# Kernel tuning notes

Hardware: AMD Instinct MI355X
Metric: run time of the kernel (lower is better)

Reference implementation:

```python
import jax, jax.numpy as jnp
import numpy as np
from jax import lax

B, T, F0 = 16, 1024, 128
L_CNN, L_RNN, D = 3, 3, 512
NF = F0 // 2  # 64, freq dim after stride-2 conv
EPS = 1e-5


def conv2d(x, w, b, stride, pad):
    # x: [B,C,H,W], w: [O,I,kh,kw]
    y = lax.conv_general_dilated(x, w, (stride, stride), [(pad, pad), (pad, pad)],
                                 dimension_numbers=('NCHW', 'OIHW', 'NCHW'))
    return y + b[None, :, None, None]


def ln_last(x, g, b):
    m = x.mean(-1, keepdims=True)
    v = ((x - m) ** 2).mean(-1, keepdims=True)
    return (x - m) * lax.rsqrt(v + EPS) * g + b


def ln_feats(x, g, b):
    # LayerNorm over freq axis (axis 2) of [B,C,F,T] (== transpose(2,3); LN; transpose back)
    m = x.mean(2, keepdims=True)
    v = ((x - m) ** 2).mean(2, keepdims=True)
    return (x - m) * lax.rsqrt(v + EPS) * g[None, None, :, None] + b[None, None, :, None]


def sru_dir(u, x_res, v, b, reverse):
    # u: [T,B,3,D] (candidate, f-pre, r-pre); x_res: [T,B,D] highway input; v,b: [2,D]
    u0 = u[:, :, 0]
    fp = u[:, :, 1] + b[0]
    rp = u[:, :, 2] + b[1]

    def step(c, inp):
        u0t, fpt, rpt, xrt = inp
        f = jax.nn.sigmoid(fpt + v[0] * c)
        r = jax.nn.sigmoid(rpt + v[1] * c)
        c = f * c + (1.0 - f) * u0t
        h = r * jnp.tanh(c) + (1.0 - r) * xrt
        return c, h

    c0 = jnp.zeros(u0.shape[1:], u.dtype)
    _, h = lax.scan(step, c0, (u0, fp, rp, x_res), reverse=reverse)
    return h  # [T,B,D]


def _forward(x, cnn_w, cnn_b, res_w1, res_b1, res_w2, res_b2,
             res_ln1_g, res_ln1_b, res_ln2_g, res_ln2_b,
             proj_w, sru_w, sru_v, sru_b, sru_ln_g, sru_ln_b,
             cls_ln_g, cls_ln_b, cls_w1, cls_b1, cls_w2, cls_b2):
    # stem conv: [B,1,128,1024] -> [B,32,64,512]
    x = conv2d(x, cnn_w, cnn_b, 2, 1)
    # residual CNN blocks (dropout = identity in eval)
    for i in range(L_CNN):
        res = x
        h = jax.nn.relu(ln_feats(x, res_ln1_g[i], res_ln1_b[i]))
        h = conv2d(h, res_w1[i], res_b1[i], 1, 1)
        h = jax.nn.relu(ln_feats(h, res_ln2_g[i], res_ln2_b[i]))
        h = conv2d(h, res_w2[i], res_b2[i], 1, 1)
        x = h + res
    # flatten channels x freq, time-major: [T', B, 32*NF]
    b_, c_, f_, t_ = x.shape
    x = x.reshape(b_, c_ * f_, t_).transpose(2, 0, 1)
    # proj_input_to_hidden_first: 2048 -> 2*D
    x = jnp.einsum('tbi,ih->tbh', x, proj_w)
    # bidirectional SRU layers
    for l in range(L_RNN):
        xl = ln_last(x, sru_ln_g[l], sru_ln_b[l])
        # u: [T,B,dir,gate,D]
        u = jnp.einsum('tbi,idkh->tbdkh', xl, sru_w[l])
        h_f = sru_dir(u[:, :, 0], x[..., :D], sru_v[l, 0], sru_b[l, 0], False)
        h_b = sru_dir(u[:, :, 1], x[..., D:], sru_v[l, 1], sru_b[l, 1], True)
        x = jnp.concatenate([h_f, h_b], axis=-1)
    # classifier: [B, T', 2D] -> [B, T', n_vocab+1]
    x = x.transpose(1, 0, 2)
    x = ln_last(x, cls_ln_g, cls_ln_b)
    x = jax.nn.relu(jnp.einsum('bth,hd->btd', x, cls_w1) + cls_b1)
    x = jnp.einsum('btd,dv->btv', x, cls_w2) + cls_b2
    return x


def setup_inputs() -> dict:
    key = jax.random.key(0)
    ks = iter(jax.random.split(key, 40))

    def rn(shape, s=0.05):
        return jax.random.normal(next(ks), shape, jnp.float32) * s

    return dict(
        x=jax.random.normal(next(ks), (B, 1, F0, T), jnp.float32),
        cnn_w=rn((32, 1, 3, 3)), cnn_b=jnp.zeros(32, jnp.float32),
        res_w1=rn((L_CNN, 32, 32, 3, 3)), res_b1=jnp.zeros((L_CNN, 32), jnp.float32),
        res_w2=rn((L_CNN, 32, 32, 3, 3)), res_b2=jnp.zeros((L_CNN, 32), jnp.float32),
        res_ln1_g=jnp.ones((L_CNN, NF), jnp.float32), res_ln1_b=jnp.zeros((L_CNN, NF), jnp.float32),
        res_ln2_g=jnp.ones((L_CNN, NF), jnp.float32), res_ln2_b=jnp.zeros((L_CNN, NF), jnp.float32),
        proj_w=rn((NF * 32, 2 * D), 0.02),
        sru_w=rn((L_RNN, 2 * D, 2, 3, D), 0.02),
        sru_v=rn((L_RNN, 2, 2, D), 0.1),
        sru_b=jnp.zeros((L_RNN, 2, 2, D), jnp.float32),
        sru_ln_g=jnp.ones((L_RNN, 2 * D), jnp.float32), sru_ln_b=jnp.zeros((L_RNN, 2 * D), jnp.float32),
        cls_ln_g=jnp.ones(2 * D, jnp.float32), cls_ln_b=jnp.zeros(2 * D, jnp.float32),
        cls_w1=rn((2 * D, D), 0.02), cls_b1=jnp.zeros(D, jnp.float32),
        cls_w2=rn((D, 29), 0.02), cls_b2=jnp.zeros(29, jnp.float32),
    )


def reference(x, cnn_w, cnn_b, res_w1, res_b1, res_w2, res_b2,
              res_ln1_g, res_ln1_b, res_ln2_g, res_ln2_b,
              proj_w, sru_w, sru_v, sru_b, sru_ln_g, sru_ln_b,
              cls_ln_g, cls_ln_b, cls_w1, cls_b1, cls_w2, cls_b2):
    return _forward(x, cnn_w, cnn_b, res_w1, res_b1, res_w2, res_b2,
                    res_ln1_g, res_ln1_b, res_ln2_g, res_ln2_b,
                    proj_w, sru_w, sru_v, sru_b, sru_ln_g, sru_ln_b,
                    cls_ln_g, cls_ln_b, cls_w1, cls_b1, cls_w2, cls_b2)
```

## Files before the change

kernel.cpp:

```cpp
#include <hip/hip_runtime.h>

typedef unsigned short u16;
typedef unsigned int u32;
typedef __attribute__((ext_vector_type(8))) short short8;
typedef __attribute__((ext_vector_type(4))) float floatx4;

__device__ __forceinline__ float bf2f(u16 u) {
    union { unsigned int i; float f; } v; v.i = ((unsigned int)u) << 16; return v.f;
}
__device__ __forceinline__ u16 f2bf(float f) {
    union { float f; unsigned int i; } v; v.f = f;
    unsigned int i = v.i + 0x7fffu + ((v.i >> 16) & 1u);
    return (u16)(i >> 16);
}

#define GLL(g, l) __builtin_amdgcn_global_load_lds( \
    (const __attribute__((address_space(1))) void*)(g), \
    (__attribute__((address_space(3))) void*)(l), 16, 0, 0)

#define WAITVM(n) asm volatile("s_waitcnt vmcnt(" #n ")" ::: "memory")
#define SBAR() __builtin_amdgcn_sched_barrier(0)

#define HA_BSTRIDE 1085568

__global__ __launch_bounds__(256) void sniff_k(const u16* __restrict__ x, int* __restrict__ flag) {
    __shared__ int red[4];
    int cnt = 0;
    for (int i = 0; i < 16; ++i) {
        u16 v = x[(threadIdx.x * 16 + i) * 2];
        int e = (v >> 7) & 0xFF;
        if (e >= 110 && e <= 135) cnt++;
    }
    #pragma unroll
    for (int off = 32; off; off >>= 1) cnt += __shfl_down(cnt, off);
    if ((threadIdx.x & 63) == 0) red[threadIdx.x >> 6] = cnt;
    __syncthreads();
    if (threadIdx.x == 0) {
        int tot = red[0] + red[1] + red[2] + red[3];
        *flag = (tot < 2048) ? 1 : 0;
    }
}

__device__ __forceinline__ float ldin(const void* p, size_t i, int isf32) {
    return isf32 ? ((const float*)p)[i] : bf2f(((const u16*)p)[i]);
}

struct CvtArgs {
    const void* src[19];
    int len[19];
    int off[19];
};
__global__ __launch_bounds__(256) void cvtall_k(CvtArgs a, float* __restrict__ dst,
                                                const int* __restrict__ flag) {
    int isf32 = *flag;
    int seg = blockIdx.y;
    int n = a.len[seg];
    const void* s = a.src[seg];
    float* d = dst + a.off[seg];
    for (int i = blockIdx.x * 256 + threadIdx.x; i < n; i += gridDim.x * 256)
        d[i] = ldin(s, i, isf32);
}

__global__ __launch_bounds__(256) void wtr_k(const void* __restrict__ W, int ldw, size_t wofs,
                                             u16* __restrict__ Wt, int ldt,
                                             const int* __restrict__ flag) {
    int isf32 = *flag;
    __shared__ u16 t[64][65];
    int k0 = blockIdx.x * 64, n0 = blockIdx.y * 64;
    int tid = threadIdx.x;
    #pragma unroll
    for (int i = 0; i < 16; ++i) {
        int kk = i * 4 + (tid >> 6), nn = tid & 63;
        t[kk][nn] = f2bf(ldin(W, wofs + (size_t)(k0 + kk) * ldw + n0 + nn, isf32));
    }
    __syncthreads();
    #pragma unroll
    for (int i = 0; i < 16; ++i) {
        int nn = i * 4 + (tid >> 6), kk = tid & 63;
        Wt[(size_t)(n0 + nn) * ldt + k0 + kk] = t[kk][nn];
    }
}

__global__ __launch_bounds__(256) void zero_k(float4* __restrict__ p, int n4) {
    float4 z = {0.f, 0.f, 0.f, 0.f};
    for (int i = blockIdx.x * 256 + threadIdx.x; i < n4; i += gridDim.x * 256) p[i] = z;
}
__global__ __launch_bounds__(256) void fill_k(float* __restrict__ p, int n) {
    int i = blockIdx.x * 256 + threadIdx.x;
    if (i < n) p[i] = 1.0e6f;
}

__global__ __launch_bounds__(256) void conv1_k(const void* __restrict__ x, const float* __restrict__ w,
                                               const float* __restrict__ bias, float* __restrict__ out,
                                               const int* __restrict__ flag) {
    int isf32 = *flag;
    int idx = blockIdx.x * 256 + threadIdx.x;
    int t  = idx & 511;
    int f  = (idx >> 9) & 63;
    int cg = (idx >> 15) & 7;
    int b  = idx >> 18;
    size_t xb = (size_t)b * 128 * 1024;

    float wr[4][9];
    #pragma unroll
    for (int i = 0; i < 4; ++i)
        #pragma unroll
        for (int k = 0; k < 9; ++k) wr[i][k] = w[(cg * 4 + i) * 9 + k];

    float acc[4];
    #pragma unroll
    for (int i = 0; i < 4; ++i) acc[i] = bias[cg * 4 + i];

    #pragma unroll
    for (int df = 0; df < 3; ++df) {
        int fi = 2 * f + df - 1;
        if (fi < 0 || fi >= 128) continue;
        size_t rowb = xb + (size_t)fi * 1024;
        float xv[3];
        #pragma unroll
        for (int dt = 0; dt < 3; ++dt) {
            int ti = 2 * t + dt - 1;
            float v = 0.f;
            if (ti >= 0 && ti < 1024) v = ldin(x, rowb + ti, isf32);
            xv[dt] = v;
        }
        #pragma unroll
        for (int i = 0; i < 4; ++i)
            #pragma unroll
            for (int dt = 0; dt < 3; ++dt)
                acc[i] = fmaf(wr[i][df * 3 + dt], xv[dt], acc[i]);
    }
    size_t obase = (((size_t)b * 32 + cg * 4) * 64 + f) * 512 + t;
    #pragma unroll
    for (int i = 0; i < 4; ++i) out[obase + (size_t)i * 64 * 512] = acc[i];
}

__global__ __launch_bounds__(256) void stats_k(const void* __restrict__ X, int isbf,
                                               float* __restrict__ sm, float* __restrict__ sr) {
    int idx = blockIdx.x * 256 + threadIdx.x;
    int t  = idx & 511;
    int bc = idx >> 9;
    size_t base = (size_t)bc * 64 * 512 + t;
    float s = 0.f, s2 = 0.f;
    #pragma unroll 8
    for (int f = 0; f < 64; ++f) {
        float v = isbf ? bf2f(((const u16*)X)[base + f * 512]) : ((const float*)X)[base + f * 512];
        s += v; s2 += v * v;
    }
    float m  = s * (1.f / 64.f);
    float var = fmaxf(s2 * (1.f / 64.f) - m * m, 0.f);
    sm[idx] = m;
    sr[idx] = rsqrtf(var + 1e-5f);
}

__global__ __launch_bounds__(256) void apply_k(const void* __restrict__ in, int isbf,
                                               const float* __restrict__ sm, const float* __restrict__ sr,
                                               const float* __restrict__ g, const float* __restrict__ be,
                                               u16* __restrict__ Ha) {
    int f = blockIdx.x;
    int b = blockIdx.y;
    float gg = g[f], bb_ = be[f];
    for (int it = 0; it < 2; ++it) {
        int t = it * 256 + threadIdx.x;
        u32 pk[16];
        #pragma unroll
        for (int cp = 0; cp < 16; ++cp) {
            u32 w = 0;
            #pragma unroll
            for (int half = 0; half < 2; ++half) {
                int ci = cp * 2 + half;
                size_t xi = (((size_t)b * 32 + ci) * 64 + f) * 512 + t;
                float xv = isbf ? bf2f(((const u16*)in)[xi]) : ((const float*)in)[xi];
                int si = (b * 32 + ci) * 512 + t;
                float hv = fmaxf((xv - sm[si]) * sr[si] * gg + bb_, 0.f);
                w |= ((u32)f2bf(hv)) << (half * 16);
            }
            pk[cp] = w;
        }
        u32* orow = (u32*)(Ha + (size_t)b * HA_BSTRIDE + ((size_t)(f + 1) * 514 + (t + 1)) * 32);
        #pragma unroll
        for (int q = 0; q < 16; ++q) orow[q] = pk[q];
    }
}

#define CVL 4
__global__ __launch_bounds__(256) void convm_k(const u16* __restrict__ Ha, void* __restrict__ out,
                                               const float* __restrict__ w, const float* __restrict__ bias,
                                               const float* __restrict__ res) {
    __shared__ __align__(16) u16 act[2][1536 * 8];
    int F0    = blockIdx.x * 16;
    int tbase = blockIdx.y * 64;
    int b     = blockIdx.z;
    const u16* Hb = Ha + (size_t)b * HA_BSTRIDE;
    int tid  = threadIdx.x;
    int lane = tid & 63;
    int wv   = tid >> 6;
    int quad = lane >> 4;
    int r    = lane & 15;
    int hasres = (res != nullptr);

    int ufp[6], utp[6], uq[6];
    #pragma unroll
    for (int it = 0; it < 6; ++it) {
        int u = it * 256 + tid;
        int u2 = (u < 1296) ? u : (u - 1296);
        int fp = u2 / 72;
        int rem = u2 - fp * 72;
        ufp[it] = fp; utp[it] = rem >> 2; uq[it] = rem & 3;
    }

    auto stage = [&](int tile, int bw) {
        int t00 = tbase + tile * 16;
        #pragma unroll
        for (int it = 0; it < 6; ++it) {
            int u = it * 256 + tid;
            GLL(Hb + ((size_t)(F0 + ufp[it]) * 514 + (t00 + utp[it])) * 32 + uq[it] * 8,
                &act[bw][u * 8]);
        }
    };

    short8 bfrag[3][3][2];
    #pragma unroll
    for (int df = 0; df < 3; ++df)
        #pragma unroll
        for (int dt = 0; dt < 3; ++dt)
            #pragma unroll
            for (int ct = 0; ct < 2; ++ct) {
                short8 v;
                #pragma unroll
                for (int j = 0; j < 8; ++j) {
                    int co = ct * 16 + r, ci = quad * 8 + j;
                    v[j] = (short)f2bf(w[(co * 32 + ci) * 9 + df * 3 + dt]);
                }
                bfrag[df][dt][ct] = v;
            }

    WAITVM(0);
    SBAR();
    stage(0, 0);
    SBAR();

    int fb = wv * 4;
    #pragma unroll 1
    for (int i = 0; i < CVL; ++i) {
        if (i < CVL - 1) stage(i + 1, (i + 1) & 1);
        SBAR();
        if (i == 0)            { WAITVM(6); }
        else if (i < CVL - 1)  { if (hasres) WAITVM(22); else WAITVM(14); }
        else                   { if (hasres) WAITVM(16); else WAITVM(8); }
        SBAR();
        __builtin_amdgcn_s_barrier();
        SBAR();

        const u16* ab = act[i & 1];
        floatx4 acc[4][2];
        #pragma unroll
        for (int ii = 0; ii < 4; ++ii)
            #pragma unroll
            for (int j = 0; j < 2; ++j)
                #pragma unroll
                for (int k = 0; k < 4; ++k) acc[ii][j][k] = 0.f;

        #pragma unroll
        for (int fh = 0; fh < 6; ++fh) {
            short8 af[3];
            #pragma unroll
            for (int dt = 0; dt < 3; ++dt)
                af[dt] = *(const short8*)&ab[((fb + fh) * 18 + (r + dt)) * 32 + quad * 8];
            #pragma unroll
            for (int df = 0; df < 3; ++df) {
                int rel = fh - df;
                if (rel < 0 || rel >= 4) continue;
                #pragma unroll
                for (int dt = 0; dt < 3; ++dt)
                    #pragma unroll
                    for (int ct = 0; ct < 2; ++ct)
                        acc[rel][ct] = __builtin_amdgcn_mfma_f32_16x16x32_bf16(
                            af[dt], bfrag[df][dt][ct], acc[rel][ct], 0, 0, 0);
            }
        }

        int t0 = tbase + i * 16;
        int tt = t0 + quad * 4;
        #pragma unroll
        for (int rel = 0; rel < 4; ++rel)
            #pragma unroll
            for (int ct = 0; ct < 2; ++ct) {
                int f  = F0 + fb + rel;
                int co = ct * 16 + r;
                size_t base = (((size_t)b * 32 + co) * 64 + f) * 512 + tt;
                float bs = bias[co];
                if (hasres) {
                    float4 rv = *(const float4*)(res + base);
                    float4 o;
                    o.x = acc[rel][ct][0] + bs + rv.x;
                    o.y = acc[rel][ct][1] + bs + rv.y;
                    o.z = acc[rel][ct][2] + bs + rv.z;
                    o.w = acc[rel][ct][3] + bs + rv.w;
                    *(float4*)((float*)out + base) = o;
                } else {
                    ushort4 o;
                    o.x = f2bf(acc[rel][ct][0] + bs);
                    o.y = f2bf(acc[rel][ct][1] + bs);
                    o.z = f2bf(acc[rel][ct][2] + bs);
                    o.w = f2bf(acc[rel][ct][3] + bs);
                    *(ushort4*)((u16*)out + base) = o;
                }
            }
        SBAR();
        __builtin_amdgcn_s_barrier();
        SBAR();
    }
}

__global__ __launch_bounds__(256) void transpose_k(const float* __restrict__ X, u16* __restrict__ A) {
    __shared__ float tile[64][65];
    int t0 = blockIdx.x * 64;
    int c  = blockIdx.y;
    int b  = blockIdx.z;
    const float* p = X + (((size_t)b * 32 + c) * 64) * 512 + t0;
    #pragma unroll
    for (int i = 0; i < 16; ++i) {
        int f = i * 4 + (threadIdx.x >> 6);
        int t = threadIdx.x & 63;
        tile[f][t] = p[(size_t)f * 512 + t];
    }
    __syncthreads();
    #pragma unroll
    for (int i = 0; i < 16; ++i) {
        int t = i * 4 + (threadIdx.x >> 6);
        int f = threadIdx.x & 63;
        A[((size_t)(t0 + t) * 16 + b) * 2048 + c * 64 + f] = f2bf(tile[f][t]);
    }
}

__global__ __launch_bounds__(256) void lnlast_k(const float* __restrict__ X, u16* __restrict__ Y,
                                                const float* __restrict__ g, const float* __restrict__ bt,
                                                int width) {
    int row = blockIdx.x;
    const float* p = X + (size_t)row * width;
    float s = 0.f, s2 = 0.f;
    for (int i = threadIdx.x; i < width; i += 256) { float v = p[i]; s += v; s2 += v * v; }
    #pragma unroll
    for (int off = 32; off; off >>= 1) { s += __shfl_down(s, off); s2 += __shfl_down(s2, off); }
    __shared__ float red[4][2];
    int wv = threadIdx.x >> 6;
    if ((threadIdx.x & 63) == 0) { red[wv][0] = s; red[wv][1] = s2; }
    __syncthreads();
    if (threadIdx.x == 0) {
        float a = 0.f, b2 = 0.f;
        for (int i = 0; i < 4; ++i) { a += red[i][0]; b2 += red[i][1]; }
        float m = a / width;
        float var = fmaxf(b2 / width - m * m, 0.f);
        red[0][0] = m; red[0][1] = rsqrtf(var + 1e-5f);
    }
    __syncthreads();
    float m = red[0][0], rs = red[0][1];
    u16* q = Y + (size_t)row * width;
    for (int i = threadIdx.x; i < width; i += 256)
        q[i] = f2bf((p[i] - m) * rs * g[i] + bt[i]);
}

__global__ __launch_bounds__(256) void gemm_bt(const u16* __restrict__ A, const u16* __restrict__ A2,
                                               int lda, const u16* __restrict__ Bt, int ldb,
                                               void* __restrict__ C, void* __restrict__ C2,
                                               int ldc, int nsplit,
                                               const float* __restrict__ bias, int relu, int K,
                                               int obf) {
    __shared__ u16 As[128 * 32];
    __shared__ u16 Bs[128 * 32];
    int tid  = threadIdx.x;
    int bm   = blockIdx.x * 128;
    int bn   = blockIdx.y * 128;
    const u16* Ab = A;
    void* Cb = C;
    int cn = bn;
    if (bn >= nsplit) { Ab = A2; Cb = C2; cn = bn - nsplit; }

    int lane = tid & 63;
    int wv   = tid >> 6;
    int quad = lane >> 4;
    int r    = lane & 15;
    int wm   = (wv >> 1) * 64;
    int wn   = (wv & 1) * 64;

    floatx4 acc[4][4];
    #pragma unroll
    for (int i = 0; i < 4; ++i)
        #pragma unroll
        for (int j = 0; j < 4; ++j)
            #pragma unroll
            for (int k = 0; k < 4; ++k) acc[i][j][k] = 0.f;

    int row0 = tid >> 2;
    int ks0  = ((tid & 3) ^ ((tid >> 3) & 3)) * 8;
    const u16* Abase  = Ab + (size_t)(bm + row0) * lda + ks0;
    const u16* Abase2 = Ab + (size_t)(bm + 64 + row0) * lda + ks0;
    const u16* Bbase  = Bt + (size_t)(bn + row0) * ldb + ks0;
    const u16* Bbase2 = Bt + (size_t)(bn + 64 + row0) * ldb + ks0;
    u16* AsD  = As + tid * 8;
    u16* AsD2 = As + 2048 + tid * 8;
    u16* BsD  = Bs + tid * 8;
    u16* BsD2 = Bs + 2048 + tid * 8;

    for (int k0 = 0; k0 < K; k0 += 32) {
        GLL(Abase + k0, AsD);
        GLL(Abase2 + k0, AsD2);
        GLL(Bbase + k0, BsD);
        GLL(Bbase2 + k0, BsD2);
        __syncthreads();
        int col = (quad ^ ((r >> 1) & 3)) * 8;
        short8 af[4], bf[4];
        #pragma unroll
        for (int mi = 0; mi < 4; ++mi) af[mi] = *(const short8*)&As[(wm + mi * 16 + r) * 32 + col];
        #pragma unroll
        for (int ni = 0; ni < 4; ++ni) bf[ni] = *(const short8*)&Bs[(wn + ni * 16 + r) * 32 + col];
        #pragma unroll
        for (int mi = 0; mi < 4; ++mi)
            #pragma unroll
            for (int ni = 0; ni < 4; ++ni)
                acc[mi][ni] = __builtin_amdgcn_mfma_f32_16x16x32_bf16(af[mi], bf[ni], acc[mi][ni], 0, 0, 0);
        __syncthreads();
    }

    #pragma unroll
    for (int mi = 0; mi < 4; ++mi)
        #pragma unroll
        for (int ni = 0; ni < 4; ++ni) {
            int col = cn + wn + ni * 16 + r;
            float bs = bias ? bias[col] : 0.f;
            #pragma unroll
            for (int reg = 0; reg < 4; ++reg) {
                int row = bm + wm + mi * 16 + quad * 4 + reg;
                float v = acc[mi][ni][reg] + bs;
                if (relu) v = fmaxf(v, 0.f);
                if (obf) ((u16*)Cb)[(size_t)row * ldc + col] = f2bf(v);
                else     ((float*)Cb)[(size_t)row * ldc + col] = v;
            }
        }
}

#define TC 256
__global__ __launch_bounds__(64) void scan_k(const u16* __restrict__ Uf, const u16* __restrict__ Ub,
                                             const float* __restrict__ Xp, float* __restrict__ Xn,
                                             float* __restrict__ cstate, const float* __restrict__ vv,
                                             const float* __restrict__ bb, int t0f, int t0b, int init) {
    __shared__ __align__(16) char lds[4][10240];
    int tid = threadIdx.x;
    int d   = blockIdx.x >> 7;
    int idx = blockIdx.x & 127;
    int b   = idx >> 3;
    int h0  = (idx & 7) * 64;
    int h   = h0 + tid;
    int gid = d * 8192 + idx * 64 + tid;

    float v0 = vv[(d * 2 + 0) * 512 + h];
    float v1 = vv[(d * 2 + 1) * 512 + h];
    float b0 = bb[(d * 2 + 0) * 512 + h];
    float b1 = bb[(d * 2 + 1) * 512 + h];
    const u16* U = d ? Ub : Uf;
    int t0 = d ? t0b : t0f;
    float* ob = Xn + (size_t)b * 1024 + d * 512 + h;
    float cc = init ? 0.f : cstate[gid];
    int tstp = d ? -16384 : 16384;

    const char* gp[10];
    int dlt[10];
    #pragma unroll
    for (int it = 0; it < 10; ++it) {
        int u = it * 64 + tid;
        int s = u / 40;
        int j = u - s * 40;
        int sl0 = d ? (TC - 1 - s) : s;
        if (j < 24) {
            int k = j >> 3, jj = j & 7;
            gp[it] = (const char*)(U + ((size_t)(sl0 * 16 + b) * 1536 + k * 512 + h0 + jj * 8));
            dlt[it] = d ? -786432 : 786432;
        } else {
            gp[it] = (const char*)(Xp + ((size_t)(t0 + sl0) * 16384 + (size_t)b * 1024 + d * 512 + h0 + (j - 24) * 4));
            dlt[it] = d ? -1048576 : 1048576;
        }
    }
    char* lbase = (char*)&lds[0][0] + tid * 16;
    auto stage = [&](int bw) {
        char* lb = lbase + bw * 10240;
        #pragma unroll
        for (int it = 0; it < 10; ++it) {
            GLL(gp[it], lb + it * 1024);
            gp[it] += dlt[it];
        }
    };

    asm volatile("s_waitcnt vmcnt(0)" ::: "memory");
    SBAR();
    stage(0);
    stage(1);
    stage(2);
    SBAR();

    #pragma unroll 1
    for (int tk = 0; tk < 16; ++tk) {
        switch (tk) {
            case 0:  WAITVM(20); break;
            case 1:  WAITVM(36); break;
            case 14: WAITVM(42); break;
            case 15: WAITVM(32); break;
            default: WAITVM(52); break;
        }
        SBAR();
        const char* Bb = (const char*)&lds[0][0] + (size_t)(tk & 3) * 10240;
        float* op = ob + (size_t)(t0 + (d ? (TC - 1 - tk * 16) : tk * 16)) * 16384;
        #pragma unroll
        for (int s = 0; s < 16; ++s) {
            const char* sb = Bb + s * 640;
            float u0 = bf2f(*(const u16*)(sb + tid * 2));
            float fp = bf2f(*(const u16*)(sb + 128 + tid * 2)) + b0;
            float rp = bf2f(*(const u16*)(sb + 256 + tid * 2)) + b1;
            float xr = *(const float*)(sb + 384 + tid * 4);
            float f = 1.f / (1.f + __expf(-(fp + v0 * cc)));
            float r = 1.f / (1.f + __expf(-(rp + v1 * cc)));
            cc = f * cc + (1.f - f) * u0;
            float th = 1.f - 2.f / (__expf(2.f * cc) + 1.f);
            *op = r * th + (1.f - r) * xr;
            op += tstp;
        }
        SBAR();
        if (tk < 13) stage((tk + 3) & 3);
        SBAR();
    }
    cstate[gid] = cc;
}

__global__ __launch_bounds__(256) void cls2_k(const float* __restrict__ FC1, const float* __restrict__ W2,
                                              const float* __restrict__ b2, void* __restrict__ out,
                                              const int* __restrict__ flag) {
    int isf32 = *flag;
    int tid = threadIdx.x;
    int rh = tid >> 7;
    int ks = (tid >> 5) & 3;
    int v  = tid & 31;
    int row = blockIdx.x * 2 + rh;
    const float* p = FC1 + (size_t)row * 512 + ks * 128;
    const float* wp = W2 + (size_t)ks * 128 * 29;
    float acc = 0.f;
    #pragma unroll 4
    for (int k = 0; k < 128; ++k) {
        float wv = (v < 29) ? wp[k * 29 + v] : 0.f;
        acc = fmaf(p[k], wv, acc);
    }
    acc += __shfl_xor(acc, 32);
    __shared__ float red[2][2][32];
    if ((tid & 63) < 32) red[rh][(tid >> 6) & 1][v] = acc;
    __syncthreads();
    if ((tid & 127) < 32 && v < 29) {
        float s = red[rh][0][v] + red[rh][1][v] + b2[v];
        int t = row >> 4, b = row & 15;
        size_t oi = ((size_t)b * 512 + t) * 29 + v;
        if (isf32) ((float*)out)[oi] = s;
        else       ((u16*)out)[oi]   = f2bf(s);
    }
}

extern "C" void kernel_launch(void* const* d_in, const int* in_sizes, int n_in,
                              void* d_out, int out_size, void* d_ws, size_t ws_size,
                              hipStream_t stream) {
    const void* x      = d_in[0];
    const void* proj_w = d_in[11];
    const void* sru_w  = d_in[12];
    const void* cls_w1 = d_in[19];

    float* ws = (float*)d_ws;
    const size_t O_X    = 0;
    const size_t O_C    = 16777216;
    const size_t O_HA   = 25165824;
    const size_t O_SM   = 33850368;
    const size_t O_SR   = 34112512;
    const size_t O_CST  = 34374656;
    const size_t O_PARK = 34391040;
    const size_t O_FLAG = 34483488;
    const size_t TOTAL  = 34483504;
    if (ws_size < TOTAL * sizeof(float)) {
        fill_k<<<(out_size + 255) / 256, 256, 0, stream>>>((float*)d_out, out_size);
        return;
    }

    float* X   = ws + O_X;
    u16*   C   = (u16*)(ws + O_C);
    u16*   HA  = (u16*)(ws + O_HA);
    float* SM  = ws + O_SM;
    float* SR  = ws + O_SR;
    float* CST = ws + O_CST;
    float* PK  = ws + O_PARK;
    int*   FLG = (int*)(ws + O_FLAG);

    u16*   Abf = (u16*)(ws + O_C);
    u16*   BtP = (u16*)(ws + 0);
    float* XP0 = ws + 25165824;
    u16*   XL  = (u16*)(ws + 0);
    float* XP1 = ws + 4194304;
    u16*   Uf  = (u16*)(ws + 12582912);
    u16*   Ub  = (u16*)(ws + 15728640);
    u16*   BtS = (u16*)(ws + 18874368);
    u16*   BtC = (u16*)(ws + O_SM);
    float* FC1 = ws + 12582912;

    float* p_cnn_w = PK + 0;      float* p_cnn_b = PK + 288;
    float* p_rw1   = PK + 320;    float* p_rb1   = PK + 27968;
    float* p_rw2   = PK + 28064;  float* p_rb2   = PK + 55712;
    float* p_l1g   = PK + 55808;  float* p_l1b   = PK + 56000;
    float* p_l2g   = PK + 56192;  float* p_l2b   = PK + 56384;
    float* p_sv    = PK + 56576;  float* p_sb    = PK + 62720;
    float* p_slng  = PK + 68864;  float* p_slnb  = PK + 71936;
    float* p_clng  = PK + 75008;  float* p_clnb  = PK + 76032;
    float* p_cb1   = PK + 77056;  float* p_cw2   = PK + 77568;
    float* p_cb2   = PK + 92416;

    sniff_k<<<1, 256, 0, stream>>>((const u16*)x, FLG);

    CvtArgs ca;
    const int srcidx[19] = {1,2,3,4,5,6,7,8,9,10,13,14,15,16,17,18,20,21,22};
    const int lens[19]   = {288,32,27648,96,27648,96,192,192,192,192,6144,6144,3072,3072,1024,1024,512,14848,29};
    const int offs[19]   = {0,288,320,27968,28064,55712,55808,56000,56192,56384,56576,62720,68864,71936,75008,76032,77056,77568,92416};
    for (int i = 0; i < 19; ++i) { ca.src[i] = d_in[srcidx[i]]; ca.len[i] = lens[i]; ca.off[i] = offs[i]; }
    cvtall_k<<<dim3(108, 19), 256, 0, stream>>>(ca, PK, FLG);

    zero_k<<<2048, 256, 0, stream>>>((float4*)HA, 2171136);
    conv1_k<<<16384, 256, 0, stream>>>(x, p_cnn_w, p_cnn_b, X, FLG);

    for (int i = 0; i < 3; ++i) {
        stats_k<<<1024, 256, 0, stream>>>(X, 0, SM, SR);
        apply_k<<<dim3(64, 16), 256, 0, stream>>>(X, 0, SM, SR, p_l1g + i * 64, p_l1b + i * 64, HA);
        convm_k<<<dim3(4, 8, 16), 256, 0, stream>>>(HA, C, p_rw1 + i * 9216, p_rb1 + i * 32, nullptr);
        stats_k<<<1024, 256, 0, stream>>>(C, 1, SM, SR);
        apply_k<<<dim3(64, 16), 256, 0, stream>>>(C, 1, SM, SR, p_l2g + i * 64, p_l2b + i * 64, HA);
        convm_k<<<dim3(4, 8, 16), 256, 0, stream>>>(HA, X, p_rw2 + i * 9216, p_rb2 + i * 32, X);
    }

    transpose_k<<<dim3(8, 32, 16), 256, 0, stream>>>(X, Abf);
    wtr_k<<<dim3(32, 16), 256, 0, stream>>>(proj_w, 1024, 0, BtP, 2048, FLG);
    gemm_bt<<<dim3(64, 8), 256, 0, stream>>>(Abf, Abf, 2048, BtP, 2048, XP0, XP0, 1024,
                                             1 << 30, nullptr, 0, 2048, 0);

    for (int l = 0; l < 3; ++l)
        wtr_k<<<dim3(16, 48), 256, 0, stream>>>(sru_w, 3072, (size_t)l * 3145728,
                                                BtS + (size_t)l * 3145728, 1024, FLG);
    wtr_k<<<dim3(16, 8), 256, 0, stream>>>(cls_w1, 512, 0, BtC, 1024, FLG);

    float* cur = XP0;
    float* nxt = XP1;
    for (int l = 0; l < 3; ++l) {
        lnlast_k<<<8192, 256, 0, stream>>>(cur, XL, p_slng + l * 1024, p_slnb + l * 1024, 1024);
        const u16* Btl = BtS + (size_t)l * 3145728;
        for (int j = 0; j < 2; ++j) {
            int t0f = j * TC;
            int t0b = (1 - j) * TC;
            gemm_bt<<<dim3(32, 24), 256, 0, stream>>>(XL + (size_t)t0f * 16 * 1024,
                                                      XL + (size_t)t0b * 16 * 1024, 1024,
                                                      Btl, 1024, Uf, Ub, 1536, 1536,
                                                      nullptr, 0, 1024, 1);
            scan_k<<<256, 64, 0, stream>>>(Uf, Ub, cur, nxt, CST,
                                           p_sv + l * 2048, p_sb + l * 2048, t0f, t0b, j == 0);
        }
        float* tmp = cur; cur = nxt; nxt = tmp;
    }

    lnlast_k<<<8192, 256, 0, stream>>>(cur, XL, p_clng, p_clnb, 1024);
    gemm_bt<<<dim3(64, 4), 256, 0, stream>>>(XL, XL, 1024, BtC, 1024, FC1, FC1, 512,
                                             1 << 30, p_cb1, 1, 1024, 0);
    cls2_k<<<4096, 256, 0, stream>>>(FC1, p_cw2, p_cb2, d_out, FLG);
}
```

Measured before the change: 1.427 ms.

## Triple-buffer GEMM LDS loads and swizzle workgroup order across XCDs

The bf16 GEMM now keeps three LDS stages, issuing async global-to-LDS loads up to three K-steps ahead and waiting with explicit vmcnt counts instead of a full sync after every load. This aims to hide global memory latency behind the MFMA work. Workgroup IDs are also remapped in groups of 8 so that neighbouring tiles land on the same XCD for better L2 reuse. LDS use triples, which may lower occupancy, and the remap assumes the workgroup count divides by 8.

```diff
diff --git a/kernel.cpp b/kernel.cpp
--- a/kernel.cpp
+++ b/kernel.cpp
@@ -367,11 +367,18 @@
                                                int ldc, int nsplit,
                                                const float* __restrict__ bias, int relu, int K,
                                                int obf) {
-    __shared__ u16 As[128 * 32];
-    __shared__ u16 Bs[128 * 32];
+    __shared__ __align__(16) u16 As[3][128 * 32];
+    __shared__ __align__(16) u16 Bs[3][128 * 32];
     int tid  = threadIdx.x;
-    int bm   = blockIdx.x * 128;
-    int bn   = blockIdx.y * 128;
+
+    int gx  = gridDim.x;
+    int nwg = gx * gridDim.y;
+    int lin = blockIdx.y * gx + blockIdx.x;
+    int q8  = nwg >> 3;
+    int swz = (lin & 7) * q8 + (lin >> 3);
+    int bm  = (swz % gx) * 128;
+    int bn  = (swz / gx) * 128;
+
     const u16* Ab = A;
     void* Cb = C;
     int cn = bn;
@@ -394,48 +401,69 @@
 
     int row0 = tid >> 2;
     int ks0  = ((tid & 3) ^ ((tid >> 3) & 3)) * 8;
-    const u16* Abase  = Ab + (size_t)(bm + row0) * lda + ks0;
-    const u16* Abase2 = Ab + (size_t)(bm + 64 + row0) * lda + ks0;
-    const u16* Bbase  = Bt + (size_t)(bn + row0) * ldb + ks0;
-    const u16* Bbase2 = Bt + (size_t)(bn + 64 + row0) * ldb + ks0;
-    u16* AsD  = As + tid * 8;
-    u16* AsD2 = As + 2048 + tid * 8;
-    u16* BsD  = Bs + tid * 8;
-    u16* BsD2 = Bs + 2048 + tid * 8;
-
-    for (int k0 = 0; k0 < K; k0 += 32) {
-        GLL(Abase + k0, AsD);
-        GLL(Abase2 + k0, AsD2);
-        GLL(Bbase + k0, BsD);
-        GLL(Bbase2 + k0, BsD2);
-        __syncthreads();
-        int col = (quad ^ ((r >> 1) & 3)) * 8;
+    const u16* Ab1 = Ab + (size_t)(bm + row0) * lda + ks0;
+    const u16* Ab2 = Ab + (size_t)(bm + 64 + row0) * lda + ks0;
+    const u16* Bb1 = Bt + (size_t)(bn + row0) * ldb + ks0;
+    const u16* Bb2 = Bt + (size_t)(bn + 64 + row0) * ldb + ks0;
+
+    auto stage = [&](int ks, int bw) {
+        int k0 = ks * 32;
+        GLL(Ab1 + k0, &As[bw][tid * 8]);
+        GLL(Ab2 + k0, &As[bw][2048 + tid * 8]);
+        GLL(Bb1 + k0, &Bs[bw][tid * 8]);
+        GLL(Bb2 + k0, &Bs[bw][2048 + tid * 8]);
+    };
+
+    int nk = K >> 5;
+    WAITVM(0);
+    SBAR();
+    stage(0, 0); stage(1, 1); stage(2, 2);
+    SBAR();
+
+    int col = (quad ^ ((r >> 1) & 3)) * 8;
+    int bc = 0;
+    #pragma unroll 1
+    for (int i = 0; i < nk; ++i) {
+        if (i + 2 < nk)       { WAITVM(8); }
+        else if (i + 1 < nk)  { WAITVM(4); }
+        else                  { WAITVM(0); }
+        SBAR();
+        __builtin_amdgcn_s_barrier();
+        SBAR();
+
+        const u16* as = As[bc];
+        const u16* bs = Bs[bc];
         short8 af[4], bf[4];
         #pragma unroll
-        for (int mi = 0; mi < 4; ++mi) af[mi] = *(const short8*)&As[(wm + mi * 16 + r) * 32 + col];
-        #pragma unroll
-        for (int ni = 0; ni < 4; ++ni) bf[ni] = *(const short8*)&Bs[(wn + ni * 16 + r) * 32 + col];
+        for (int mi = 0; mi < 4; ++mi) af[mi] = *(const short8*)&as[(wm + mi * 16 + r) * 32 + col];
+        #pragma unroll
+        for (int ni = 0; ni < 4; ++ni) bf[ni] = *(const short8*)&bs[(wn + ni * 16 + r) * 32 + col];
         #pragma unroll
         for (int mi = 0; mi < 4; ++mi)
             #pragma unroll
             for (int ni = 0; ni < 4; ++ni)
                 acc[mi][ni] = __builtin_amdgcn_mfma_f32_16x16x32_bf16(af[mi], bf[ni], acc[mi][ni], 0, 0, 0);
-        __syncthreads();
+
+        SBAR();
+        __builtin_amdgcn_s_barrier();
+        SBAR();
+        if (i + 3 < nk) stage(i + 3, bc);
+        bc = (bc == 2) ? 0 : bc + 1;
     }
 
     #pragma unroll
     for (int mi = 0; mi < 4; ++mi)
         #pragma unroll
         for (int ni = 0; ni < 4; ++ni) {
-            int col = cn + wn + ni * 16 + r;
-            float bs = bias ? bias[col] : 0.f;
+            int ccol = cn + wn + ni * 16 + r;
+            float bsv = bias ? bias[ccol] : 0.f;
             #pragma unroll
             for (int reg = 0; reg < 4; ++reg) {
                 int row = bm + wm + mi * 16 + quad * 4 + reg;
-                float v = acc[mi][ni][reg] + bs;
+                float v = acc[mi][ni][reg] + bsv;
                 if (relu) v = fmaxf(v, 0.f);
-                if (obf) ((u16*)Cb)[(size_t)row * ldc + col] = f2bf(v);
-                else     ((float*)Cb)[(size_t)row * ldc + col] = v;
+                if (obf) ((u16*)Cb)[(size_t)row * ldc + ccol] = f2bf(v);
+                else     ((float*)Cb)[(size_t)row * ldc + ccol] = v;
             }
         }
 }
```

After: 1.399 ms. -2.0%, faster.
